# Kernel tuning notes

Measured on AMD Instinct MI355X. Metric: run time of the kernel, lower is better.

Reference implementation:

```python
import jax, jax.numpy as jnp
import numpy as np

F_IN, HID, F_OUT = 8, 64, 8
R, C = 256, 4096
NUM_SETS, N_IND, M = 3, 4096, 4096


def setup_inputs() -> dict:
    key = jax.random.key(0)
    k0, k1, k2 = jax.random.split(key, 3)
    input_tensor = jax.random.normal(k0, (F_IN, R, C), dtype=jnp.float32)
    w1 = jax.random.normal(k1, (HID, 3 * F_IN), dtype=jnp.float32) * 0.1
    b1 = jnp.zeros((HID,), jnp.float32)
    w2 = jax.random.normal(k2, (F_OUT, HID), dtype=jnp.float32) * 0.1
    b2 = jnp.zeros((F_OUT,), jnp.float32)
    rng = np.random.default_rng(0)
    def make_ind():
        # col0: permutation of [0, N_IND) (duplicate-free scatter-set destinations)
        # col1: random source column in [0, C)
        col0 = np.stack([rng.permutation(N_IND) for _ in range(NUM_SETS)])
        col1 = rng.integers(0, C, size=(NUM_SETS, N_IND))
        return jnp.asarray(np.stack([col0, col1], axis=-1), jnp.int32)
    ind0, ind1, ind2 = make_ind(), make_ind(), make_ind()
    mix_ind = jnp.asarray(rng.integers(0, N_IND, size=(NUM_SETS, 3, M)), jnp.int32)
    return {"input_tensor": input_tensor, "w1": w1, "b1": b1, "w2": w2, "b2": b2,
            "ind0": ind0, "ind1": ind1, "ind2": ind2, "mix_ind": mix_ind}


def reference(input_tensor, w1, b1, w2, b2, ind0, ind1, ind2, mix_ind):
    # Output for row r depends only on input row r, so we process all R at once
    # (the original chunk loop over R is pure tiling).
    F_in, Rr, Cc = input_tensor.shape
    F_out = w2.shape[0]
    num_sets = ind0.shape[0]

    def project(ind, mi):
        # res[..., ind[:,0]] = input[..., ind[:,1]]; then take slots mi -> [F_in, R, M]
        n = ind.shape[0]
        res = jnp.zeros((F_in, Rr, n), input_tensor.dtype)
        res = res.at[..., ind[:, 0]].set(input_tensor[..., ind[:, 1]])
        return res[..., mi]

    out_rcf = jnp.zeros((Rr, Cc, F_out), input_tensor.dtype)  # zeros = include_self baseline
    for s in range(num_sets):
        c1 = project(ind0[s], mix_ind[s, 0])
        c2 = project(ind1[s], mix_ind[s, 1])
        c3 = project(ind2[s], mix_ind[s, 2])
        c = jnp.concatenate([c1, c2, c3], axis=0)          # [3F_in, R, M]
        c_flat = c.transpose(1, 2, 0).reshape(-1, 3 * F_in)  # [R*M, 3F_in]
        a1 = jax.nn.relu(c_flat @ w1.T + b1)                 # [R*M, HID]
        d = (a1 @ w2.T + b2).reshape(Rr, -1, F_out)          # [R, M, F_out]
        for i, ind in enumerate((ind0[s], ind1[s], ind2[s])):
            idx = ind[:, 1][mix_ind[s, i]]                   # [M] target columns in C
            out_rcf = out_rcf.at[:, idx, :].max(d)           # amax scatter, include_self
    return out_rcf.transpose(2, 0, 1)                        # [F_out, R, C]
```

## Files before the change

kernel.cpp:

```cpp
#include <hip/hip_runtime.h>
#include <cstdint>

#define F_IN   8
#define HID    64
#define F_OUTD 8
#define RDIM   256
#define CDIM   4096
#define NSETS  3
#define NIND   4096
#define MDIM   4096
#define MAXL   64
#define GC     16
#define MPW    4

using short8 = __attribute__((ext_vector_type(8))) short;
using f32x4  = __attribute__((ext_vector_type(4))) float;

__device__ inline unsigned int cvtpk(float a, float b) {
    unsigned int r;
    asm("v_cvt_pk_bf16_f32 %0, %1, %2" : "=v"(r) : "v"(a), "v"(b));
    return r;
}
__device__ inline unsigned int pkmaxu(unsigned int a, unsigned int b) {
    unsigned int r;
    asm("v_pk_max_u16 %0, %1, %2" : "=v"(r) : "v"(a), "v"(b));
    return r;
}

__global__ __launch_bounds__(256)
void prep_in(const float* __restrict__ in, unsigned short* __restrict__ out) {
    const int PADH = 264;
    __shared__ unsigned short tile[32 * PADH];
    int c0 = blockIdx.x * 32, r0 = blockIdx.y * 32;
    int t = threadIdx.x;
    int tx = t & 31, ty = t >> 5;
#pragma unroll
    for (int f = 0; f < 8; f += 2)
#pragma unroll
        for (int rr = 0; rr < 4; rr++) {
            int r = ty + rr * 8;
            float v0 = in[((size_t)f * RDIM + (r0 + r)) * CDIM + c0 + tx];
            float v1 = in[((size_t)(f + 1) * RDIM + (r0 + r)) * CDIM + c0 + tx];
            *(unsigned int*)&tile[tx * PADH + r * 8 + f] = cvtpk(v0, v1);
        }
    __syncthreads();
    int r = t & 31, cl = t >> 5;
#pragma unroll
    for (int cc = 0; cc < 4; cc++) {
        int c = cc * 8 + cl;
        uint4 v = *(const uint4*)&tile[c * PADH + r * 8];
        *(uint4*)(out + (((size_t)(c0 + c) * RDIM) + (r0 + r)) * 8) = v;
    }
}

__global__ void build_inv(const int* __restrict__ ind0, const int* __restrict__ ind1,
                          const int* __restrict__ ind2,
                          const float* __restrict__ w1, const float* __restrict__ w2,
                          int* __restrict__ inv, int* __restrict__ mergecnt,
                          unsigned short* __restrict__ w1bf, unsigned short* __restrict__ w2bf) {
    int k  = blockIdx.x * 256 + threadIdx.x;
    int si = blockIdx.y;
    int s_ = si / 3, i_ = si % 3;
    const int* ind = (i_ == 0 ? ind0 : (i_ == 1 ? ind1 : ind2)) + (size_t)s_ * NIND * 2;
    int c0 = ind[2 * k];
    inv[(size_t)si * NIND + c0] = k;
    if (si == 0) mergecnt[k] = 0;
    if (blockIdx.x == 0 && blockIdx.y == 0) {
        int t = threadIdx.x;
        for (int i = t; i < 64 * 32; i += 256) {
            int j = i >> 5, kk = i & 31;
            w1bf[i] = (kk < 24) ? (unsigned short)(cvtpk(w1[j * 24 + kk], 0.f) & 0xffff) : 0;
        }
        for (int i = t; i < 16 * 64; i += 256) {
            int f = i >> 6, kg = i & 63;
            int hi = kg >> 5, q = (kg >> 3) & 3, e = kg & 7;
            int j = (hi << 5) + ((e >> 2) << 4) + (q << 2) + (e & 3);
            w2bf[i] = (f < 8) ? (unsigned short)(cvtpk(w2[f * 64 + j], 0.f) & 0xffff) : 0;
        }
    }
}

__global__ void build_buckets(const int* __restrict__ ind0, const int* __restrict__ ind1,
                              const int* __restrict__ ind2, const int* __restrict__ mix,
                              int* __restrict__ mergecnt, int* __restrict__ mergelist) {
    int m  = blockIdx.x * 256 + threadIdx.x;
    int si = blockIdx.y;
    int s_ = si / 3, i_ = si % 3;
    const int* ind = (i_ == 0 ? ind0 : (i_ == 1 ? ind1 : ind2)) + (size_t)s_ * NIND * 2;
    int mi = mix[(size_t)si * MDIM + m];
    int c  = ind[2 * mi + 1];
    int slot = atomicAdd(&mergecnt[c], 1);
    if (slot < MAXL) mergelist[(size_t)c * MAXL + slot] = s_ * MDIM + m;
}

__global__ __launch_bounds__(256, 2)
void mlp_store(const unsigned short* __restrict__ inT2,
               const unsigned short* __restrict__ w1bf,
               const unsigned short* __restrict__ w2bf,
               const float* __restrict__ b1, const float* __restrict__ b2,
               const int* __restrict__ ind0, const int* __restrict__ ind1,
               const int* __restrict__ ind2, const int* __restrict__ mix,
               const int* __restrict__ inv,
               unsigned short* __restrict__ dbuf) {
    int t    = threadIdx.x;
    int wave = t >> 6, lane = t & 63;
    int lo = lane & 15, q = lane >> 4;

    int wid  = blockIdx.x * 4 + wave;
    int mgrp = wid & 1023;
    int half = (wid >> 10) & 1;
    int s_   = wid >> 11;
    int m0   = mgrp * MPW;

    short8 A1[4], A2[2];
#pragma unroll
    for (int tt = 0; tt < 4; tt++)
        A1[tt] = *(const short8*)(w1bf + ((16 * tt + lo) << 5) + (q << 3));
#pragma unroll
    for (int kk = 0; kk < 2; kk++)
        A2[kk] = *(const short8*)(w2bf + (lo << 6) + (kk << 5) + (q << 3));

    f32x4 bbv[4];
#pragma unroll
    for (int tt = 0; tt < 4; tt++)
#pragma unroll
        for (int rg = 0; rg < 4; rg++)
            bbv[tt][rg] = b1[16 * tt + 4 * q + rg];
    f32x4 b2f;
#pragma unroll
    for (int rg = 0; rg < 4; rg++) {
        int f = 4 * q + rg;
        b2f[rg] = (f < 8) ? b2[f] : 0.f;
    }

    int gq[MPW] = {0, 0, 0, 0};
    if (q < 3) {
        int si = s_ * 3 + q;
        const int* indq = (q == 0 ? ind0 : (q == 1 ? ind1 : ind2)) + (size_t)s_ * NIND * 2;
        int mi[MPW], kk[MPW];
#pragma unroll
        for (int u = 0; u < MPW; u++) mi[u] = mix[(size_t)si * MDIM + m0 + u];
#pragma unroll
        for (int u = 0; u < MPW; u++) kk[u] = inv[(size_t)si * NIND + mi[u]];
#pragma unroll
        for (int u = 0; u < MPW; u++) gq[u] = indq[2 * kk[u] + 1];
    }
    const unsigned short* srcs[MPW];
#pragma unroll
    for (int u = 0; u < MPW; u++)
        srcs[u] = inT2 + ((size_t)gq[u] * RDIM + half * 128 + lo) * 8;

    unsigned short* dst = dbuf + (size_t)(s_ * MDIM + m0) * 2048 + half * 1024 + lo * 8 + q * 4;

    union U { unsigned int u[4]; short8 s; };
    const short8 zero8 = {0, 0, 0, 0, 0, 0, 0, 0};

    short8 Bcur = zero8;
    if (q < 3) Bcur = *(const short8*)srcs[0];
#pragma unroll
    for (int it = 0; it < MPW * 8; it++) {
        const int u = it >> 3, j = it & 7;
        short8 Bnext = Bcur;
        if (it < MPW * 8 - 1 && q < 3)
            Bnext = *(const short8*)(srcs[(it + 1) >> 3] + ((it + 1) & 7) * 128);

        f32x4 a0 = __builtin_amdgcn_mfma_f32_16x16x32_bf16(A1[0], Bcur, bbv[0], 0, 0, 0);
        f32x4 a1 = __builtin_amdgcn_mfma_f32_16x16x32_bf16(A1[1], Bcur, bbv[1], 0, 0, 0);
        f32x4 a2 = __builtin_amdgcn_mfma_f32_16x16x32_bf16(A1[2], Bcur, bbv[2], 0, 0, 0);
        f32x4 a3 = __builtin_amdgcn_mfma_f32_16x16x32_bf16(A1[3], Bcur, bbv[3], 0, 0, 0);

        U ba, bb;
        ba.u[0] = cvtpk(fmaxf(a0[0], 0.f), fmaxf(a0[1], 0.f));
        ba.u[1] = cvtpk(fmaxf(a0[2], 0.f), fmaxf(a0[3], 0.f));
        ba.u[2] = cvtpk(fmaxf(a1[0], 0.f), fmaxf(a1[1], 0.f));
        ba.u[3] = cvtpk(fmaxf(a1[2], 0.f), fmaxf(a1[3], 0.f));
        bb.u[0] = cvtpk(fmaxf(a2[0], 0.f), fmaxf(a2[1], 0.f));
        bb.u[1] = cvtpk(fmaxf(a2[2], 0.f), fmaxf(a2[3], 0.f));
        bb.u[2] = cvtpk(fmaxf(a3[0], 0.f), fmaxf(a3[1], 0.f));
        bb.u[3] = cvtpk(fmaxf(a3[2], 0.f), fmaxf(a3[3], 0.f));

        f32x4 o = __builtin_amdgcn_mfma_f32_16x16x32_bf16(A2[0], ba.s, b2f, 0, 0, 0);
        o = __builtin_amdgcn_mfma_f32_16x16x32_bf16(A2[1], bb.s, o, 0, 0, 0);

        if (q < 2) {
            uint2 ov;
            ov.x = cvtpk(fmaxf(o[0], 0.f), fmaxf(o[1], 0.f));
            ov.y = cvtpk(fmaxf(o[2], 0.f), fmaxf(o[3], 0.f));
            *(uint2*)(dst + (size_t)u * 2048 + j * 128) = ov;
        }
        Bcur = Bnext;
    }
}

__global__ __launch_bounds__(256)
void gather_max_t(const unsigned short* __restrict__ dbuf, const int* __restrict__ mergecnt,
                  const int* __restrict__ mergelist, float* __restrict__ out) {
    __shared__ float ldsT[8][16][20];
    __shared__ int   mlist[GC][MAXL];
    int c0 = blockIdx.x * GC;
    int t  = threadIdx.x;
    int tc = t >> 4, tr = t & 15;
    int c  = c0 + tc;

    int n = mergecnt[c]; if (n > MAXL) n = MAXL;
    for (int e = tr; e < n; e += 16)
        mlist[tc][e] = mergelist[(size_t)c * MAXL + e];
    __syncthreads();

    uint4 acc[4];
#pragma unroll
    for (int p = 0; p < 4; p++) acc[p] = make_uint4(0u, 0u, 0u, 0u);

    int rbase = blockIdx.y * 64 + tr;
    if (n > 0) {
        const unsigned short* bp = dbuf + ((size_t)mlist[tc][0] * RDIM + rbase) * 8;
        uint4 p0 = *(const uint4*)(bp);
        uint4 p1 = *(const uint4*)(bp + 16 * 8);
        uint4 p2 = *(const uint4*)(bp + 32 * 8);
        uint4 p3 = *(const uint4*)(bp + 48 * 8);
        for (int e = 1; e < n; e++) {
            const unsigned short* bq = dbuf + ((size_t)mlist[tc][e] * RDIM + rbase) * 8;
            uint4 q0 = *(const uint4*)(bq);
            uint4 q1 = *(const uint4*)(bq + 16 * 8);
            uint4 q2 = *(const uint4*)(bq + 32 * 8);
            uint4 q3 = *(const uint4*)(bq + 48 * 8);
            acc[0].x = pkmaxu(acc[0].x, p0.x); acc[0].y = pkmaxu(acc[0].y, p0.y);
            acc[0].z = pkmaxu(acc[0].z, p0.z); acc[0].w = pkmaxu(acc[0].w, p0.w);
            acc[1].x = pkmaxu(acc[1].x, p1.x); acc[1].y = pkmaxu(acc[1].y, p1.y);
            acc[1].z = pkmaxu(acc[1].z, p1.z); acc[1].w = pkmaxu(acc[1].w, p1.w);
            acc[2].x = pkmaxu(acc[2].x, p2.x); acc[2].y = pkmaxu(acc[2].y, p2.y);
            acc[2].z = pkmaxu(acc[2].z, p2.z); acc[2].w = pkmaxu(acc[2].w, p2.w);
            acc[3].x = pkmaxu(acc[3].x, p3.x); acc[3].y = pkmaxu(acc[3].y, p3.y);
            acc[3].z = pkmaxu(acc[3].z, p3.z); acc[3].w = pkmaxu(acc[3].w, p3.w);
            p0 = q0; p1 = q1; p2 = q2; p3 = q3;
        }
        acc[0].x = pkmaxu(acc[0].x, p0.x); acc[0].y = pkmaxu(acc[0].y, p0.y);
        acc[0].z = pkmaxu(acc[0].z, p0.z); acc[0].w = pkmaxu(acc[0].w, p0.w);
        acc[1].x = pkmaxu(acc[1].x, p1.x); acc[1].y = pkmaxu(acc[1].y, p1.y);
        acc[1].z = pkmaxu(acc[1].z, p1.z); acc[1].w = pkmaxu(acc[1].w, p1.w);
        acc[2].x = pkmaxu(acc[2].x, p2.x); acc[2].y = pkmaxu(acc[2].y, p2.y);
        acc[2].z = pkmaxu(acc[2].z, p2.z); acc[2].w = pkmaxu(acc[2].w, p2.w);
        acc[3].x = pkmaxu(acc[3].x, p3.x); acc[3].y = pkmaxu(acc[3].y, p3.y);
        acc[3].z = pkmaxu(acc[3].z, p3.z); acc[3].w = pkmaxu(acc[3].w, p3.w);
    }

#pragma unroll
    for (int p = 0; p < 4; p++) {
        if (p) __syncthreads();
        ldsT[0][tr][tc] = __uint_as_float(acc[p].x << 16);
        ldsT[1][tr][tc] = __uint_as_float(acc[p].x & 0xffff0000u);
        ldsT[2][tr][tc] = __uint_as_float(acc[p].y << 16);
        ldsT[3][tr][tc] = __uint_as_float(acc[p].y & 0xffff0000u);
        ldsT[4][tr][tc] = __uint_as_float(acc[p].z << 16);
        ldsT[5][tr][tc] = __uint_as_float(acc[p].z & 0xffff0000u);
        ldsT[6][tr][tc] = __uint_as_float(acc[p].w << 16);
        ldsT[7][tr][tc] = __uint_as_float(acc[p].w & 0xffff0000u);
        __syncthreads();
#pragma unroll
        for (int k2 = 0; k2 < 2; k2++) {
            int idx2 = t * 2 + k2;
            int f = idx2 >> 6, rl = (idx2 >> 2) & 15, cq = idx2 & 3;
            *(float4*)&out[((size_t)f * RDIM + blockIdx.y * 64 + p * 16 + rl) * CDIM + c0 + cq * 4] =
                *(const float4*)&ldsT[f][rl][cq * 4];
        }
    }
}

extern "C" void kernel_launch(void* const* d_in, const int* in_sizes, int n_in,
                              void* d_out, int out_size, void* d_ws, size_t ws_size,
                              hipStream_t stream) {
    const float* input = (const float*)d_in[0];
    const float* w1    = (const float*)d_in[1];
    const float* b1    = (const float*)d_in[2];
    const float* w2    = (const float*)d_in[3];
    const float* b2    = (const float*)d_in[4];
    const int*   ind0  = (const int*)d_in[5];
    const int*   ind1  = (const int*)d_in[6];
    const int*   ind2  = (const int*)d_in[7];
    const int*   mix   = (const int*)d_in[8];

    const size_t MiB = 1ull << 20;
    char* ws = (char*)d_ws;
    unsigned short* inT2 = (unsigned short*)ws;
    unsigned short* dbuf = (unsigned short*)(ws + 16 * MiB);
    char* tail = ws + 64 * MiB;
    int* inv       = (int*)tail;
    int* mergecnt  = (int*)(tail + 147456);
    int* mergelist = (int*)(tail + 147456 + 16384);
    unsigned short* w1bf = (unsigned short*)(tail + 147456 + 16384 + (size_t)CDIM * MAXL * 4);
    unsigned short* w2bf = w1bf + 64 * 32;

    prep_in<<<dim3(CDIM / 32, RDIM / 32), 256, 0, stream>>>(input, inT2);
    build_inv<<<dim3(NIND / 256, 9), 256, 0, stream>>>(ind0, ind1, ind2, w1, w2,
                                                       inv, mergecnt, w1bf, w2bf);
    build_buckets<<<dim3(MDIM / 256, 9), 256, 0, stream>>>(ind0, ind1, ind2, mix,
                                                           mergecnt, mergelist);
    mlp_store<<<NSETS * 2 * (MDIM / MPW) / 4, 256, 0, stream>>>(inT2, w1bf, w2bf, b1, b2,
                                                                ind0, ind1, ind2, mix, inv, dbuf);
    gather_max_t<<<dim3(CDIM / GC, 4), 256, 0, stream>>>(dbuf, mergecnt, mergelist,
                                                         (float*)d_out);
}
```

Before: 88.28 us.

## Restructure gather-max to one wave per column with 1024-thread blocks

The final gather/max kernel now uses 1024 threads per block, one wavefront per output column and one lane per row. Each thread loads a single uint4 per merge entry instead of four, which raises thread-level parallelism and memory-level concurrency for the bucket gather. The LDS transpose is reworked to store packed bf16 pairs and write two feature planes per thread with a single barrier, and it adds index clamping and a relu clamp on output. The trade-off is fewer independent loads in flight per thread and larger blocks, which may limit occupancy.

```diff
diff --git a/kernel.cpp b/kernel.cpp
--- a/kernel.cpp
+++ b/kernel.cpp
@@ -192,78 +192,60 @@
     }
 }
 
-__global__ __launch_bounds__(256)
+__global__ __launch_bounds__(1024)
 void gather_max_t(const unsigned short* __restrict__ dbuf, const int* __restrict__ mergecnt,
                   const int* __restrict__ mergelist, float* __restrict__ out) {
-    __shared__ float ldsT[8][16][20];
-    __shared__ int   mlist[GC][MAXL];
+    __shared__ unsigned int ldsP[4][64][20];
+    __shared__ int mlist[GC][MAXL];
+    int t = threadIdx.x;
+    int w = t >> 6, lane = t & 63;
     int c0 = blockIdx.x * GC;
-    int t  = threadIdx.x;
-    int tc = t >> 4, tr = t & 15;
-    int c  = c0 + tc;
-
-    int n = mergecnt[c]; if (n > MAXL) n = MAXL;
-    for (int e = tr; e < n; e += 16)
-        mlist[tc][e] = mergelist[(size_t)c * MAXL + e];
+    int c  = c0 + w;
+
+    mlist[w][lane] = 0;
+    int n = mergecnt[c];
+    n = n < 0 ? 0 : (n > MAXL ? MAXL : n);
+    if (lane < n) {
+        int idx = mergelist[(size_t)c * MAXL + lane];
+        idx = idx < 0 ? 0 : (idx >= NSETS * MDIM ? NSETS * MDIM - 1 : idx);
+        mlist[w][lane] = idx;
+    }
     __syncthreads();
 
-    uint4 acc[4];
-#pragma unroll
-    for (int p = 0; p < 4; p++) acc[p] = make_uint4(0u, 0u, 0u, 0u);
-
-    int rbase = blockIdx.y * 64 + tr;
+    int r = blockIdx.y * 64 + lane;
+    uint4 acc = make_uint4(0u, 0u, 0u, 0u);
     if (n > 0) {
-        const unsigned short* bp = dbuf + ((size_t)mlist[tc][0] * RDIM + rbase) * 8;
-        uint4 p0 = *(const uint4*)(bp);
-        uint4 p1 = *(const uint4*)(bp + 16 * 8);
-        uint4 p2 = *(const uint4*)(bp + 32 * 8);
-        uint4 p3 = *(const uint4*)(bp + 48 * 8);
+        uint4 p = *(const uint4*)(dbuf + ((size_t)mlist[w][0] * RDIM + r) * 8);
         for (int e = 1; e < n; e++) {
-            const unsigned short* bq = dbuf + ((size_t)mlist[tc][e] * RDIM + rbase) * 8;
-            uint4 q0 = *(const uint4*)(bq);
-            uint4 q1 = *(const uint4*)(bq + 16 * 8);
-            uint4 q2 = *(const uint4*)(bq + 32 * 8);
-            uint4 q3 = *(const uint4*)(bq + 48 * 8);
-            acc[0].x = pkmaxu(acc[0].x, p0.x); acc[0].y = pkmaxu(acc[0].y, p0.y);
-            acc[0].z = pkmaxu(acc[0].z, p0.z); acc[0].w = pkmaxu(acc[0].w, p0.w);
-            acc[1].x = pkmaxu(acc[1].x, p1.x); acc[1].y = pkmaxu(acc[1].y, p1.y);
-            acc[1].z = pkmaxu(acc[1].z, p1.z); acc[1].w = pkmaxu(acc[1].w, p1.w);
-            acc[2].x = pkmaxu(acc[2].x, p2.x); acc[2].y = pkmaxu(acc[2].y, p2.y);
-            acc[2].z = pkmaxu(acc[2].z, p2.z); acc[2].w = pkmaxu(acc[2].w, p2.w);
-            acc[3].x = pkmaxu(acc[3].x, p3.x); acc[3].y = pkmaxu(acc[3].y, p3.y);
-            acc[3].z = pkmaxu(acc[3].z, p3.z); acc[3].w = pkmaxu(acc[3].w, p3.w);
-            p0 = q0; p1 = q1; p2 = q2; p3 = q3;
-        }
-        acc[0].x = pkmaxu(acc[0].x, p0.x); acc[0].y = pkmaxu(acc[0].y, p0.y);
-        acc[0].z = pkmaxu(acc[0].z, p0.z); acc[0].w = pkmaxu(acc[0].w, p0.w);
-        acc[1].x = pkmaxu(acc[1].x, p1.x); acc[1].y = pkmaxu(acc[1].y, p1.y);
-        acc[1].z = pkmaxu(acc[1].z, p1.z); acc[1].w = pkmaxu(acc[1].w, p1.w);
-        acc[2].x = pkmaxu(acc[2].x, p2.x); acc[2].y = pkmaxu(acc[2].y, p2.y);
-        acc[2].z = pkmaxu(acc[2].z, p2.z); acc[2].w = pkmaxu(acc[2].w, p2.w);
-        acc[3].x = pkmaxu(acc[3].x, p3.x); acc[3].y = pkmaxu(acc[3].y, p3.y);
-        acc[3].z = pkmaxu(acc[3].z, p3.z); acc[3].w = pkmaxu(acc[3].w, p3.w);
-    }
-
-#pragma unroll
-    for (int p = 0; p < 4; p++) {
-        if (p) __syncthreads();
-        ldsT[0][tr][tc] = __uint_as_float(acc[p].x << 16);
-        ldsT[1][tr][tc] = __uint_as_float(acc[p].x & 0xffff0000u);
-        ldsT[2][tr][tc] = __uint_as_float(acc[p].y << 16);
-        ldsT[3][tr][tc] = __uint_as_float(acc[p].y & 0xffff0000u);
-        ldsT[4][tr][tc] = __uint_as_float(acc[p].z << 16);
-        ldsT[5][tr][tc] = __uint_as_float(acc[p].z & 0xffff0000u);
-        ldsT[6][tr][tc] = __uint_as_float(acc[p].w << 16);
-        ldsT[7][tr][tc] = __uint_as_float(acc[p].w & 0xffff0000u);
-        __syncthreads();
-#pragma unroll
-        for (int k2 = 0; k2 < 2; k2++) {
-            int idx2 = t * 2 + k2;
-            int f = idx2 >> 6, rl = (idx2 >> 2) & 15, cq = idx2 & 3;
-            *(float4*)&out[((size_t)f * RDIM + blockIdx.y * 64 + p * 16 + rl) * CDIM + c0 + cq * 4] =
-                *(const float4*)&ldsT[f][rl][cq * 4];
-        }
-    }
+            uint4 nx = *(const uint4*)(dbuf + ((size_t)mlist[w][e] * RDIM + r) * 8);
+            acc.x = pkmaxu(acc.x, p.x); acc.y = pkmaxu(acc.y, p.y);
+            acc.z = pkmaxu(acc.z, p.z); acc.w = pkmaxu(acc.w, p.w);
+            p = nx;
+        }
+        acc.x = pkmaxu(acc.x, p.x); acc.y = pkmaxu(acc.y, p.y);
+        acc.z = pkmaxu(acc.z, p.z); acc.w = pkmaxu(acc.w, p.w);
+    }
+
+    ldsP[0][lane][w] = acc.x;
+    ldsP[1][lane][w] = acc.y;
+    ldsP[2][lane][w] = acc.z;
+    ldsP[3][lane][w] = acc.w;
+    __syncthreads();
+
+    int f2 = t >> 8, rl = (t >> 2) & 63, cq = t & 3;
+    uint4 v = *(const uint4*)&ldsP[f2][rl][cq * 4];
+    float4 lo, hi;
+    lo.x = fmaxf(__uint_as_float(v.x << 16), 0.f);
+    hi.x = fmaxf(__uint_as_float(v.x & 0xffff0000u), 0.f);
+    lo.y = fmaxf(__uint_as_float(v.y << 16), 0.f);
+    hi.y = fmaxf(__uint_as_float(v.y & 0xffff0000u), 0.f);
+    lo.z = fmaxf(__uint_as_float(v.z << 16), 0.f);
+    hi.z = fmaxf(__uint_as_float(v.z & 0xffff0000u), 0.f);
+    lo.w = fmaxf(__uint_as_float(v.w << 16), 0.f);
+    hi.w = fmaxf(__uint_as_float(v.w & 0xffff0000u), 0.f);
+    size_t rowoff = (size_t)blockIdx.y * 64 + rl;
+    *(float4*)&out[((size_t)(2 * f2) * RDIM + rowoff) * CDIM + c0 + cq * 4] = lo;
+    *(float4*)&out[((size_t)(2 * f2 + 1) * RDIM + rowoff) * CDIM + c0 + cq * 4] = hi;
 }
 
 extern "C" void kernel_launch(void* const* d_in, const int* in_sizes, int n_in,
@@ -297,6 +279,6 @@
                                                            mergecnt, mergelist);
     mlp_store<<<NSETS * 2 * (MDIM / MPW) / 4, 256, 0, stream>>>(inT2, w1bf, w2bf, b1, b2,
                                                                 ind0, ind1, ind2, mix, inv, dbuf);
-    gather_max_t<<<dim3(CDIM / GC, 4), 256, 0, stream>>>(dbuf, mergecnt, mergelist,
-                                                         (float*)d_out);
-}
+    gather_max_t<<<dim3(CDIM / GC, 4), 1024, 0, stream>>>(dbuf, mergecnt, mergelist,
+                                                          (float*)d_out);
+}
```

Result: no change. 88.31 us (+0.0%).
